# Kernel optimization log

Measured on AMD Instinct MI355X. Metric: run time of the kernel, lower is better.

The kernel has to match this reference:

```python
import jax, jax.numpy as jnp
import numpy as np

N = 100000
E = 1600000
NEG_SLOPE = 0.2


def gat_layer(x, W, al, ar, b, src, dst):
    """DGL GATConv (no dropout, no residual, bias=True, activation=None).
    x: [N, in]; W: [in, H*D]; al, ar, b: [H, D]. Returns [N, H, D]."""
    H, D = al.shape
    feat = (x @ W).reshape(N, H, D)               # [N,H,D]
    el = jnp.sum(feat * al, axis=-1)              # [N,H]
    er = jnp.sum(feat * ar, axis=-1)              # [N,H]
    e = jax.nn.leaky_relu(el[src] + er[dst], NEG_SLOPE)  # [E,H]
    # segment softmax over incoming edges of each dst node
    emax = jax.lax.stop_gradient(jax.ops.segment_max(e, dst, num_segments=N))
    ex = jnp.exp(e - emax[dst])                   # [E,H]
    denom = jax.ops.segment_sum(ex, dst, num_segments=N)  # [N,H]
    alpha = ex / jnp.where(denom[dst] == 0, 1.0, denom[dst])  # [E,H]
    msg = feat[src] * alpha[..., None]            # [E,H,D] gather + weight
    out = jax.ops.segment_sum(msg, dst, num_segments=N)    # [N,H,D] scatter-add
    return out + b[None, :, :]


def setup_inputs() -> dict:
    key = jax.random.key(0)
    ks = jax.random.split(key, 12)
    in_size, hid, out_size, heads = 128, 32, 16, 4
    x = jax.random.normal(ks[0], (N, in_size), dtype=jnp.float32)
    src = jax.random.randint(ks[1], (E,), 0, N, dtype=jnp.int32)
    dst = jax.random.randint(ks[2], (E,), 0, N, dtype=jnp.int32)
    W1 = jax.random.normal(ks[3], (in_size, heads * hid), dtype=jnp.float32) * (1.0 / np.sqrt(in_size))
    al1 = jax.random.normal(ks[4], (heads, hid), dtype=jnp.float32) * 0.1
    ar1 = jax.random.normal(ks[5], (heads, hid), dtype=jnp.float32) * 0.1
    b1 = jnp.zeros((heads, hid), dtype=jnp.float32)
    W2 = jax.random.normal(ks[6], (hid, out_size), dtype=jnp.float32) * (1.0 / np.sqrt(hid))
    al2 = jax.random.normal(ks[7], (1, out_size), dtype=jnp.float32) * 0.1
    ar2 = jax.random.normal(ks[8], (1, out_size), dtype=jnp.float32) * 0.1
    b2 = jnp.zeros((1, out_size), dtype=jnp.float32)
    return {"x": x, "src": src, "dst": dst, "W1": W1, "al1": al1, "ar1": ar1,
            "b1": b1, "W2": W2, "al2": al2, "ar2": ar2, "b2": b2}


def reference(x, src, dst, W1, al1, ar1, b1, W2, al2, ar2, b2):
    h = gat_layer(x, W1, al1, ar1, b1, src, dst)   # [N, heads, hid]
    h = jax.nn.relu(jnp.mean(h, axis=1))           # mean over heads + relu
    h = gat_layer(h, W2, al2, ar2, b2, src, dst)   # [N, 1, out]
    return h.reshape(N, -1)                        # flatten
```

## Files before the change

kernel.cpp:

```cpp
#include <hip/hip_runtime.h>
#include <hip/hip_bf16.h>

#define NEG_SLOPE 0.2f
#define LOG2E 1.44269504f
#define G_SHIFT 7
#define GSZ 128
#define CHUNK 4096

typedef __attribute__((ext_vector_type(8))) __bf16 bf16x8;
typedef __attribute__((ext_vector_type(4))) float f32x4;
typedef __attribute__((ext_vector_type(2))) float f32x2;

__device__ __forceinline__ unsigned short f2bf(float f) {
    unsigned u = __float_as_uint(f);
    unsigned r = (u + 0x7fffu + ((u >> 16) & 1u)) >> 16;
    return (unsigned short)r;
}
__device__ __forceinline__ float bflo(unsigned v) { return __uint_as_float(v << 16); }
__device__ __forceinline__ float bfhi(unsigned v) { return __uint_as_float(v & 0xffff0000u); }
__device__ __forceinline__ float bf2f(unsigned short v) {
    return __uint_as_float((unsigned)v << 16);
}

__global__ __launch_bounds__(256) void coarse_scatter(
    const int* __restrict__ src, const int* __restrict__ dst,
    int* __restrict__ gcursor, unsigned* __restrict__ inter, int NB, int E) {
    __shared__ int hist[800];
    __shared__ int lbase[800];
    __shared__ int gbase[800];
    __shared__ unsigned stage[CHUNK];
    __shared__ unsigned short bstage[CHUNK];

    const int tid = threadIdx.x;
    const int e0 = blockIdx.x * CHUNK;
    const int cnt = min(CHUNK, E - e0);

    for (int i = tid; i < NB; i += 256) hist[i] = 0;
    __syncthreads();

    unsigned pk[16];
    int bb[16];
    unsigned short rk[16];
#pragma unroll
    for (int r = 0; r < 16; ++r) {
        int idx = tid + r * 256;
        if (idx < cnt) {
            int s = src[e0 + idx];
            int d = dst[e0 + idx];
            pk[r] = ((unsigned)s << G_SHIFT) | (unsigned)(d & (GSZ - 1));
            bb[r] = d >> G_SHIFT;
            rk[r] = (unsigned short)atomicAdd(&hist[bb[r]], 1);
        }
    }
    __syncthreads();
    if (tid < 64) {
        int carry = 0;
        for (int i = 0; i < NB; i += 64) {
            int v = (i + tid < NB) ? hist[i + tid] : 0;
            int xv = v;
            for (int o = 1; o < 64; o <<= 1) {
                int tt = __shfl_up(xv, o, 64);
                if (tid >= o) xv += tt;
            }
            if (i + tid < NB) lbase[i + tid] = carry + xv - v;
            carry += __shfl(xv, 63, 64);
        }
    }
    __syncthreads();
    for (int i = tid; i < NB; i += 256) {
        int hh = hist[i];
        gbase[i] = (hh > 0) ? (i * CHUNK + atomicAdd(&gcursor[i], hh)) : 0;
    }
    __syncthreads();
#pragma unroll
    for (int r = 0; r < 16; ++r) {
        int idx = tid + r * 256;
        if (idx < cnt) {
            int pos = lbase[bb[r]] + (int)rk[r];
            stage[pos] = pk[r];
            bstage[pos] = (unsigned short)bb[r];
        }
    }
    __syncthreads();
#pragma unroll
    for (int r = 0; r < 16; ++r) {
        int idx = tid + r * 256;
        if (idx < cnt) {
            int b = (int)bstage[idx];
            inter[gbase[b] + (idx - lbase[b])] = stage[idx];
        }
    }
}

__global__ __launch_bounds__(256) void fine_scatter(
    const unsigned* __restrict__ inter, const int* __restrict__ gcursor,
    int* __restrict__ deg, int* __restrict__ rowptr, int* __restrict__ esrc,
    int N, int NB) {
    __shared__ int h[GSZ];
    __shared__ int lb[GSZ];
    __shared__ int redsum[256];
    const int b = blockIdx.x;
    const int tid = threadIdx.x;
    const int cnt = gcursor[b];
    const unsigned* ep = inter + (size_t)b * CHUNK;

    {
        int s = 0;
        for (int i = tid; i < b; i += 256) s += gcursor[i];
        redsum[tid] = s;
        __syncthreads();
        for (int o = 128; o > 0; o >>= 1) {
            if (tid < o) redsum[tid] += redsum[tid + o];
            __syncthreads();
        }
    }
    const int base = redsum[0];

    if (tid < GSZ) h[tid] = 0;
    __syncthreads();

    for (int idx = tid; idx < cnt; idx += 256)
        atomicAdd(&h[(int)(ep[idx] & (GSZ - 1))], 1);
    __syncthreads();

    if (tid < 64) {
        int carry = 0;
        for (int i = 0; i < GSZ; i += 64) {
            int v = h[i + tid];
            int xv = v;
            for (int o = 1; o < 64; o <<= 1) {
                int tt = __shfl_up(xv, o, 64);
                if (tid >= o) xv += tt;
            }
            lb[i + tid] = carry + xv - v;
            carry += __shfl(xv, 63, 64);
        }
    }
    __syncthreads();
    if (tid < GSZ) {
        int node = b * GSZ + tid;
        if (node < N) {
            deg[node] = h[tid];
            rowptr[node] = base + lb[tid];
        }
        h[tid] = 0;
    }
    __syncthreads();

    int* eb = esrc + base;
    for (int idx = tid; idx < cnt; idx += 256) {
        unsigned ed = ep[idx];
        int l = (int)(ed & (GSZ - 1));
        int rk = atomicAdd(&h[l], 1);
        eb[lb[l] + rk] = (int)(ed >> G_SHIFT);
    }
}

__global__ __launch_bounds__(128) void wconv_kernel(
    const float* __restrict__ W, unsigned short* __restrict__ wtb) {
    int c = blockIdx.x;
    int k = threadIdx.x;
    wtb[c * 128 + k] = f2bf(W[k * 128 + c]);
}

#define GSTRIDE 136
__global__ __launch_bounds__(256) void gemm1_mfma(
    const float* __restrict__ x, const unsigned short* __restrict__ wtb,
    const float* __restrict__ al, const float* __restrict__ ar,
    unsigned short* __restrict__ featb, float* __restrict__ el,
    float* __restrict__ er, int N) {
    __shared__ unsigned short xs[128][GSTRIDE];
    __shared__ unsigned short ws[128][GSTRIDE];
    const int t = threadIdx.x;
    const int m0 = blockIdx.x * 128;
    const int w = t >> 6;
    const int l = t & 63;
    const int lr = l & 15;
    const int lg = l >> 4;

    {
        const uint4* wv = (const uint4*)wtb;
#pragma unroll
        for (int rr = 0; rr < 8; ++rr) {
            int q = t + 256 * rr;
            int c = q >> 4, kb = q & 15;
            uint4 v = wv[q];
            *((uint4*)&ws[c][kb * 8]) = v;
        }
    }
    {
#pragma unroll
        for (int rr = 0; rr < 16; ++rr) {
            int q = t + 256 * rr;
            int row = q >> 5, c4 = q & 31;
            int gm = m0 + row;
            if (gm >= N) gm = N - 1;
            float4 v = *((const float4*)(x + (size_t)gm * 128 + c4 * 4));
            ushort4 o;
            o.x = f2bf(v.x); o.y = f2bf(v.y); o.z = f2bf(v.z); o.w = f2bf(v.w);
            *((ushort4*)&xs[row][c4 * 4]) = o;
        }
    }
    __syncthreads();

    f32x4 acc[2][8];
#pragma unroll
    for (int i = 0; i < 2; ++i)
#pragma unroll
        for (int j = 0; j < 8; ++j) acc[i][j] = (f32x4){0.f, 0.f, 0.f, 0.f};

#pragma unroll
    for (int kk = 0; kk < 4; ++kk) {
        const int k0 = kk * 32 + lg * 8;
        bf16x8 a0 = *((const bf16x8*)&xs[w * 32 + lr][k0]);
        bf16x8 a1 = *((const bf16x8*)&xs[w * 32 + 16 + lr][k0]);
#pragma unroll
        for (int nj = 0; nj < 8; ++nj) {
            bf16x8 bfr = *((const bf16x8*)&ws[nj * 16 + lr][k0]);
            acc[0][nj] = __builtin_amdgcn_mfma_f32_16x16x32_bf16(a0, bfr, acc[0][nj], 0, 0, 0);
            acc[1][nj] = __builtin_amdgcn_mfma_f32_16x16x32_bf16(a1, bfr, acc[1][nj], 0, 0, 0);
        }
    }
    __syncthreads();
#pragma unroll
    for (int mi = 0; mi < 2; ++mi)
#pragma unroll
        for (int r = 0; r < 4; ++r) {
            int row = w * 32 + mi * 16 + lg * 4 + r;
#pragma unroll
            for (int nj = 0; nj < 8; ++nj)
                xs[row][nj * 16 + lr] = f2bf(acc[mi][nj][r]);
        }
    __syncthreads();
    {
        int row = t >> 1, half = t & 1;
        int gm = m0 + row;
        if (gm < N) {
            float pl0 = 0.f, pl1 = 0.f, pr0 = 0.f, pr1 = 0.f;
            const unsigned short* xr = &xs[row][half * 64];
            uint4* outp = (uint4*)(featb + (size_t)gm * 128 + half * 64);
#pragma unroll
            for (int b8 = 0; b8 < 8; ++b8) {
                uint4 v = *((const uint4*)(xr + b8 * 8));
                int cb = half * 64 + b8 * 8;
                float4 a0 = *((const float4*)(al + cb));
                float4 a1 = *((const float4*)(al + cb + 4));
                float4 r0 = *((const float4*)(ar + cb));
                float4 r1 = *((const float4*)(ar + cb + 4));
                float f0 = bflo(v.x), f1 = bfhi(v.x), f2 = bflo(v.y), f3 = bfhi(v.y);
                float f4 = bflo(v.z), f5 = bfhi(v.z), f6 = bflo(v.w), f7 = bfhi(v.w);
                float sl = f0 * a0.x + f1 * a0.y + f2 * a0.z + f3 * a0.w
                         + f4 * a1.x + f5 * a1.y + f6 * a1.z + f7 * a1.w;
                float sr = f0 * r0.x + f1 * r0.y + f2 * r0.z + f3 * r0.w
                         + f4 * r1.x + f5 * r1.y + f6 * r1.z + f7 * r1.w;
                if (b8 < 4) { pl0 += sl; pr0 += sr; } else { pl1 += sl; pr1 += sr; }
                outp[b8] = v;
            }
            el[gm * 4 + half * 2 + 0] = pl0 * LOG2E;
            el[gm * 4 + half * 2 + 1] = pl1 * LOG2E;
            er[gm * 4 + half * 2 + 0] = pr0 * LOG2E;
            er[gm * 4 + half * 2 + 1] = pr1 * LOG2E;
        }
    }
}

__global__ __launch_bounds__(256) void pull1_kernel(
    const int* __restrict__ rowptr, const int* __restrict__ deg,
    const int* __restrict__ esrc, const float* __restrict__ el,
    const float* __restrict__ er, const unsigned short* __restrict__ featb,
    const float* __restrict__ b,
    const float* __restrict__ W2, const float* __restrict__ al2,
    const float* __restrict__ ar2, unsigned short* __restrict__ feat2b,
    float* __restrict__ el2, float* __restrict__ er2, int N) {
    int tid = blockIdx.x * 256 + threadIdx.x;
    int node = tid >> 4;
    int lane = threadIdx.x & 15;
    if (node >= N) return;
    int h = lane >> 2;
    int dq = lane & 3;
    int start = rowptr[node];
    int cnt = deg[node];
    float er_nh = er[node * 4 + h];
    const int* ep = esrc + start;
    const unsigned short* fb = featb + h * 32 + dq * 8;

    f32x2 acc2[4];
#pragma unroll
    for (int j = 0; j < 4; ++j) acc2[j] = (f32x2){0.f, 0.f};
    float sumex = 0.f;

    for (int i = 0; i < cnt; i += 8) {
        int s[8]; float e[8]; uint4 u[8];
#pragma unroll
        for (int j = 0; j < 8; ++j) {
            int idx = i + j;
            idx = (idx < cnt) ? idx : (cnt - 1);
            s[j] = ep[idx];
        }
#pragma unroll
        for (int j = 0; j < 8; ++j) u[j] = *((const uint4*)(fb + (size_t)s[j] * 128));
#pragma unroll
        for (int j = 0; j < 8; ++j) e[j] = el[s[j] * 4 + h];
#pragma unroll
        for (int j = 0; j < 8; ++j) {
            float v = e[j] + er_nh;
            v = fmaxf(v, NEG_SLOPE * v);
            float xx = (i + j < cnt) ? exp2f(v) : 0.f;
            sumex += xx;
            f32x2 xx2 = (f32x2){xx, xx};
            acc2[0] += xx2 * (f32x2){bflo(u[j].x), bfhi(u[j].x)};
            acc2[1] += xx2 * (f32x2){bflo(u[j].y), bfhi(u[j].y)};
            acc2[2] += xx2 * (f32x2){bflo(u[j].z), bfhi(u[j].z)};
            acc2[3] += xx2 * (f32x2){bflo(u[j].w), bfhi(u[j].w)};
        }
    }

    float inv = 1.f / ((sumex == 0.f) ? 1.f : sumex);
    float4 bb0 = *((const float4*)(b + h * 32 + dq * 8));
    float4 bb1 = *((const float4*)(b + h * 32 + dq * 8 + 4));
    float o[8];
    o[0] = acc2[0].x * inv + bb0.x; o[1] = acc2[0].y * inv + bb0.y;
    o[2] = acc2[1].x * inv + bb0.z; o[3] = acc2[1].y * inv + bb0.w;
    o[4] = acc2[2].x * inv + bb1.x; o[5] = acc2[2].y * inv + bb1.y;
    o[6] = acc2[3].x * inv + bb1.z; o[7] = acc2[3].y * inv + bb1.w;
#pragma unroll
    for (int j = 0; j < 8; ++j) {
        o[j] += __shfl_xor(o[j], 4);
        o[j] += __shfl_xor(o[j], 8);
        o[j] = fmaxf(o[j] * 0.25f, 0.f);
    }
    int c = lane;
    float fc = 0.f;
#pragma unroll
    for (int q = 0; q < 4; ++q) {
#pragma unroll
        for (int j = 0; j < 8; ++j) {
            float hv = __shfl(o[j], q, 16);
            fc += hv * W2[(q * 8 + j) * 16 + c];
        }
    }
    float pl = fc * al2[c];
    float pr = fc * ar2[c];
    pl += __shfl_xor(pl, 1); pl += __shfl_xor(pl, 2);
    pl += __shfl_xor(pl, 4); pl += __shfl_xor(pl, 8);
    pr += __shfl_xor(pr, 1); pr += __shfl_xor(pr, 2);
    pr += __shfl_xor(pr, 4); pr += __shfl_xor(pr, 8);
    feat2b[(size_t)node * 16 + c] = f2bf(fc);
    if (lane == 0) {
        el2[node] = pl * LOG2E;
        er2[node] = pr * LOG2E;
    }
}

__global__ __launch_bounds__(128) void pull2_kernel(
    const int* __restrict__ rowptr, const int* __restrict__ deg,
    const int* __restrict__ esrc, const float* __restrict__ el,
    const float* __restrict__ er, const unsigned short* __restrict__ feat2b,
    const float* __restrict__ b, float* __restrict__ outp, int N) {
    int tid = blockIdx.x * 128 + threadIdx.x;
    int node = tid >> 2;
    int d4 = threadIdx.x & 3;
    if (node >= N) return;

    int start = rowptr[node];
    int cnt = deg[node];
    float er_n = er[node];
    const int* ep = esrc + start;
    const unsigned short* fb = feat2b + d4 * 4;

    f32x2 acc01 = (f32x2){0.f, 0.f};
    f32x2 acc23 = (f32x2){0.f, 0.f};
    float sumex = 0.f;
    for (int i = 0; i < cnt; i += 8) {
        int s[8]; float ee[8]; ushort4 ff[8];
#pragma unroll
        for (int j = 0; j < 8; ++j) {
            int idx = i + j;
            idx = (idx < cnt) ? idx : (cnt - 1);
            s[j] = ep[idx];
        }
#pragma unroll
        for (int j = 0; j < 8; ++j) {
            ee[j] = el[s[j]];
            ff[j] = *((const ushort4*)(fb + (size_t)s[j] * 16));
        }
#pragma unroll
        for (int j = 0; j < 8; ++j) {
            float v = ee[j] + er_n;
            v = fmaxf(v, NEG_SLOPE * v);
            float ex = (i + j < cnt) ? exp2f(v) : 0.f;
            sumex += ex;
            f32x2 ex2 = (f32x2){ex, ex};
            acc01 += ex2 * (f32x2){bf2f(ff[j].x), bf2f(ff[j].y)};
            acc23 += ex2 * (f32x2){bf2f(ff[j].z), bf2f(ff[j].w)};
        }
    }
    float inv = 1.f / ((sumex == 0.f) ? 1.f : sumex);
    float4 bb = *((const float4*)(b + d4 * 4));
    float4 o;
    o.x = acc01.x * inv + bb.x;
    o.y = acc01.y * inv + bb.y;
    o.z = acc23.x * inv + bb.z;
    o.w = acc23.y * inv + bb.w;
    *((float4*)(outp + (size_t)node * 16 + d4 * 4)) = o;
}

extern "C" void kernel_launch(void* const* d_in, const int* in_sizes, int n_in,
                              void* d_out, int out_size, void* d_ws, size_t ws_size,
                              hipStream_t stream) {
    const float* x   = (const float*)d_in[0];
    const int*   src = (const int*)d_in[1];
    const int*   dst = (const int*)d_in[2];
    const float* W1  = (const float*)d_in[3];
    const float* al1 = (const float*)d_in[4];
    const float* ar1 = (const float*)d_in[5];
    const float* b1  = (const float*)d_in[6];
    const float* W2  = (const float*)d_in[7];
    const float* al2 = (const float*)d_in[8];
    const float* ar2 = (const float*)d_in[9];
    const float* b2  = (const float*)d_in[10];

    const int E = in_sizes[1];
    const int N = in_sizes[0] / 128;
    const int H1 = 4, C1 = 128;
    const int D2 = 16;
    const int NB = (N + GSZ - 1) / GSZ;
    const int NCH = (E + CHUNK - 1) / CHUNK;

    char* p = (char*)d_ws;
    auto alloc_f = [&](size_t n) { float* q = (float*)p; p += n * sizeof(float); return q; };
    auto alloc_i = [&](size_t n) { int* q = (int*)p; p += n * sizeof(int); return q; };

    unsigned short* feat1b = (unsigned short*)p; p += (size_t)N * C1 * sizeof(unsigned short);
    unsigned short* feat2b = (unsigned short*)p; p += (size_t)N * D2 * sizeof(unsigned short);
    float* el1   = alloc_f((size_t)N * H1);
    float* er1   = alloc_f((size_t)N * H1);
    float* el2   = alloc_f(N);
    float* er2   = alloc_f(N);
    int* deg     = alloc_i(N);
    int* rowptr  = alloc_i(N);
    int* esrc    = alloc_i(E);
    int* gcursor = alloc_i(NB);
    unsigned* inter = (unsigned*)alloc_i((size_t)NB * CHUNK);
    unsigned short* wtb = (unsigned short*)p; p += (size_t)128 * 128 * sizeof(unsigned short);

    const int TB = 256;

    hipMemsetAsync(gcursor, 0, (size_t)NB * sizeof(int), stream);
    wconv_kernel<<<128, 128, 0, stream>>>(W1, wtb);
    coarse_scatter<<<NCH, TB, 0, stream>>>(src, dst, gcursor, inter, NB, E);
    fine_scatter<<<NB, TB, 0, stream>>>(inter, gcursor, deg, rowptr, esrc, N, NB);

    gemm1_mfma<<<(N + 127) / 128, TB, 0, stream>>>(x, wtb, al1, ar1, feat1b, el1, er1, N);
    pull1_kernel<<<(int)(((long long)N * 16 + 255) / 256), TB, 0, stream>>>(
        rowptr, deg, esrc, el1, er1, feat1b, b1,
        W2, al2, ar2, feat2b, el2, er2, N);

    pull2_kernel<<<(int)(((long long)N * 4 + 127) / 128), 128, 0, stream>>>(
        rowptr, deg, esrc, el2, er2, feat2b, b2, (float*)d_out, N);
}
```

Baseline: 256.6 us.

## Merge independent preprocessing kernels and widen gather batches in pull kernels

The weight bf16 conversion moves into extra blocks of the coarse scatter kernel. The fine scatter moves into extra blocks of the GEMM kernel, which now shares one dynamic shared buffer between the two block roles. This cuts the launch count from four to two and lets independent work run concurrently. Both pull kernels now batch 16 neighbor gathers per iteration instead of 8 to raise memory-level parallelism, at the cost of more registers and more wasted clamped loads on low-degree nodes.

```diff
diff --git a/kernel.cpp b/kernel.cpp
--- a/kernel.cpp
+++ b/kernel.cpp
@@ -6,6 +6,7 @@
 #define G_SHIFT 7
 #define GSZ 128
 #define CHUNK 4096
+#define GSTRIDE 136
 
 typedef __attribute__((ext_vector_type(8))) __bf16 bf16x8;
 typedef __attribute__((ext_vector_type(4))) float f32x4;
@@ -22,9 +23,11 @@
     return __uint_as_float((unsigned)v << 16);
 }
 
-__global__ __launch_bounds__(256) void coarse_scatter(
+__global__ __launch_bounds__(256) void k1_scatter_wconv(
     const int* __restrict__ src, const int* __restrict__ dst,
-    int* __restrict__ gcursor, unsigned* __restrict__ inter, int NB, int E) {
+    int* __restrict__ gcursor, unsigned* __restrict__ inter,
+    const float* __restrict__ W, unsigned short* __restrict__ wtb,
+    int NB, int E, int NCH) {
     __shared__ int hist[800];
     __shared__ int lbase[800];
     __shared__ int gbase[800];
@@ -32,6 +35,13 @@
     __shared__ unsigned short bstage[CHUNK];
 
     const int tid = threadIdx.x;
+    if ((int)blockIdx.x >= NCH) {
+        int idx = ((int)blockIdx.x - NCH) * 256 + tid;
+        int c = idx >> 7, k = idx & 127;
+        wtb[idx] = f2bf(W[k * 128 + c]);
+        return;
+    }
+
     const int e0 = blockIdx.x * CHUNK;
     const int cnt = min(CHUNK, E - e0);
 
@@ -92,87 +102,78 @@
     }
 }
 
-__global__ __launch_bounds__(256) void fine_scatter(
+__global__ __launch_bounds__(256) void k2_fine_gemm(
     const unsigned* __restrict__ inter, const int* __restrict__ gcursor,
     int* __restrict__ deg, int* __restrict__ rowptr, int* __restrict__ esrc,
-    int N, int NB) {
-    __shared__ int h[GSZ];
-    __shared__ int lb[GSZ];
-    __shared__ int redsum[256];
-    const int b = blockIdx.x;
-    const int tid = threadIdx.x;
-    const int cnt = gcursor[b];
-    const unsigned* ep = inter + (size_t)b * CHUNK;
-
-    {
-        int s = 0;
-        for (int i = tid; i < b; i += 256) s += gcursor[i];
-        redsum[tid] = s;
-        __syncthreads();
-        for (int o = 128; o > 0; o >>= 1) {
-            if (tid < o) redsum[tid] += redsum[tid + o];
-            __syncthreads();
-        }
-    }
-    const int base = redsum[0];
-
-    if (tid < GSZ) h[tid] = 0;
-    __syncthreads();
-
-    for (int idx = tid; idx < cnt; idx += 256)
-        atomicAdd(&h[(int)(ep[idx] & (GSZ - 1))], 1);
-    __syncthreads();
-
-    if (tid < 64) {
-        int carry = 0;
-        for (int i = 0; i < GSZ; i += 64) {
-            int v = h[i + tid];
-            int xv = v;
-            for (int o = 1; o < 64; o <<= 1) {
-                int tt = __shfl_up(xv, o, 64);
-                if (tid >= o) xv += tt;
-            }
-            lb[i + tid] = carry + xv - v;
-            carry += __shfl(xv, 63, 64);
-        }
-    }
-    __syncthreads();
-    if (tid < GSZ) {
-        int node = b * GSZ + tid;
-        if (node < N) {
-            deg[node] = h[tid];
-            rowptr[node] = base + lb[tid];
-        }
-        h[tid] = 0;
-    }
-    __syncthreads();
-
-    int* eb = esrc + base;
-    for (int idx = tid; idx < cnt; idx += 256) {
-        unsigned ed = ep[idx];
-        int l = (int)(ed & (GSZ - 1));
-        int rk = atomicAdd(&h[l], 1);
-        eb[lb[l] + rk] = (int)(ed >> G_SHIFT);
-    }
-}
-
-__global__ __launch_bounds__(128) void wconv_kernel(
-    const float* __restrict__ W, unsigned short* __restrict__ wtb) {
-    int c = blockIdx.x;
-    int k = threadIdx.x;
-    wtb[c * 128 + k] = f2bf(W[k * 128 + c]);
-}
-
-#define GSTRIDE 136
-__global__ __launch_bounds__(256) void gemm1_mfma(
     const float* __restrict__ x, const unsigned short* __restrict__ wtb,
     const float* __restrict__ al, const float* __restrict__ ar,
     unsigned short* __restrict__ featb, float* __restrict__ el,
-    float* __restrict__ er, int N) {
-    __shared__ unsigned short xs[128][GSTRIDE];
-    __shared__ unsigned short ws[128][GSTRIDE];
-    const int t = threadIdx.x;
-    const int m0 = blockIdx.x * 128;
+    float* __restrict__ er, int N, int NB) {
+    __shared__ __align__(16) unsigned short smem[2 * 128 * GSTRIDE];
+    const int tid = threadIdx.x;
+
+    if ((int)blockIdx.x < NB) {
+        int* h = (int*)smem;
+        int* lb = h + GSZ;
+        int* redsum = lb + GSZ;
+        const int b = blockIdx.x;
+        const int cnt = gcursor[b];
+        const unsigned* ep = inter + (size_t)b * CHUNK;
+
+        {
+            int s = 0;
+            for (int i = tid; i < b; i += 256) s += gcursor[i];
+            redsum[tid] = s;
+            __syncthreads();
+            for (int o = 128; o > 0; o >>= 1) {
+                if (tid < o) redsum[tid] += redsum[tid + o];
+                __syncthreads();
+            }
+        }
+        const int base = redsum[0];
+
+        if (tid < GSZ) h[tid] = 0;
+        __syncthreads();
+        for (int idx = tid; idx < cnt; idx += 256)
+            atomicAdd(&h[(int)(ep[idx] & (GSZ - 1))], 1);
+        __syncthreads();
+        if (tid < 64) {
+            int carry = 0;
+            for (int i = 0; i < GSZ; i += 64) {
+                int v = h[i + tid];
+                int xv = v;
+                for (int o = 1; o < 64; o <<= 1) {
+                    int tt = __shfl_up(xv, o, 64);
+                    if (tid >= o) xv += tt;
+                }
+                lb[i + tid] = carry + xv - v;
+                carry += __shfl(xv, 63, 64);
+            }
+        }
+        __syncthreads();
+        if (tid < GSZ) {
+            int node = b * GSZ + tid;
+            if (node < N) {
+                deg[node] = h[tid];
+                rowptr[node] = base + lb[tid];
+            }
+            h[tid] = 0;
+        }
+        __syncthreads();
+        int* eb = esrc + base;
+        for (int idx = tid; idx < cnt; idx += 256) {
+            unsigned ed = ep[idx];
+            int l = (int)(ed & (GSZ - 1));
+            int rk = atomicAdd(&h[l], 1);
+            eb[lb[l] + rk] = (int)(ed >> G_SHIFT);
+        }
+        return;
+    }
+
+    unsigned short (*xs)[GSTRIDE] = (unsigned short(*)[GSTRIDE])smem;
+    unsigned short (*ws)[GSTRIDE] = (unsigned short(*)[GSTRIDE])(smem + 128 * GSTRIDE);
+    const int t = tid;
+    const int m0 = ((int)blockIdx.x - NB) * 128;
     const int w = t >> 6;
     const int l = t & 63;
     const int lr = l & 15;
@@ -289,20 +290,22 @@
     for (int j = 0; j < 4; ++j) acc2[j] = (f32x2){0.f, 0.f};
     float sumex = 0.f;
 
-    for (int i = 0; i < cnt; i += 8) {
-        int s[8]; float e[8]; uint4 u[8];
-#pragma unroll
-        for (int j = 0; j < 8; ++j) {
+    for (int i = 0; i < cnt; i += 16) {
+        int s[16];
+#pragma unroll
+        for (int j = 0; j < 16; ++j) {
             int idx = i + j;
             idx = (idx < cnt) ? idx : (cnt - 1);
             s[j] = ep[idx];
         }
-#pragma unroll
-        for (int j = 0; j < 8; ++j) u[j] = *((const uint4*)(fb + (size_t)s[j] * 128));
-#pragma unroll
-        for (int j = 0; j < 8; ++j) e[j] = el[s[j] * 4 + h];
-#pragma unroll
-        for (int j = 0; j < 8; ++j) {
+        uint4 u[16];
+#pragma unroll
+        for (int j = 0; j < 16; ++j) u[j] = *((const uint4*)(fb + (size_t)s[j] * 128));
+        float e[16];
+#pragma unroll
+        for (int j = 0; j < 16; ++j) e[j] = el[s[j] * 4 + h];
+#pragma unroll
+        for (int j = 0; j < 16; ++j) {
             float v = e[j] + er_nh;
             v = fmaxf(v, NEG_SLOPE * v);
             float xx = (i + j < cnt) ? exp2f(v) : 0.f;
@@ -371,21 +374,22 @@
     f32x2 acc01 = (f32x2){0.f, 0.f};
     f32x2 acc23 = (f32x2){0.f, 0.f};
     float sumex = 0.f;
-    for (int i = 0; i < cnt; i += 8) {
-        int s[8]; float ee[8]; ushort4 ff[8];
-#pragma unroll
-        for (int j = 0; j < 8; ++j) {
+    for (int i = 0; i < cnt; i += 16) {
+        int s[16];
+#pragma unroll
+        for (int j = 0; j < 16; ++j) {
             int idx = i + j;
             idx = (idx < cnt) ? idx : (cnt - 1);
             s[j] = ep[idx];
         }
-#pragma unroll
-        for (int j = 0; j < 8; ++j) {
-            ee[j] = el[s[j]];
-            ff[j] = *((const ushort4*)(fb + (size_t)s[j] * 16));
-        }
-#pragma unroll
-        for (int j = 0; j < 8; ++j) {
+        ushort4 ff[16];
+#pragma unroll
+        for (int j = 0; j < 16; ++j) ff[j] = *((const ushort4*)(fb + (size_t)s[j] * 16));
+        float ee[16];
+#pragma unroll
+        for (int j = 0; j < 16; ++j) ee[j] = el[s[j]];
+#pragma unroll
+        for (int j = 0; j < 16; ++j) {
             float v = ee[j] + er_n;
             v = fmaxf(v, NEG_SLOPE * v);
             float ex = (i + j < cnt) ? exp2f(v) : 0.f;
@@ -426,6 +430,7 @@
     const int D2 = 16;
     const int NB = (N + GSZ - 1) / GSZ;
     const int NCH = (E + CHUNK - 1) / CHUNK;
+    const int GB = (N + 127) / 128;
 
     char* p = (char*)d_ws;
     auto alloc_f = [&](size_t n) { float* q = (float*)p; p += n * sizeof(float); return q; };
@@ -447,11 +452,13 @@
     const int TB = 256;
 
     hipMemsetAsync(gcursor, 0, (size_t)NB * sizeof(int), stream);
-    wconv_kernel<<<128, 128, 0, stream>>>(W1, wtb);
-    coarse_scatter<<<NCH, TB, 0, stream>>>(src, dst, gcursor, inter, NB, E);
-    fine_scatter<<<NB, TB, 0, stream>>>(inter, gcursor, deg, rowptr, esrc, N, NB);
-
-    gemm1_mfma<<<(N + 127) / 128, TB, 0, stream>>>(x, wtb, al1, ar1, feat1b, el1, er1, N);
+    k1_scatter_wconv<<<NCH + 64, TB, 0, stream>>>(
+        src, dst, gcursor, inter, W1, wtb, NB, E, NCH);
+
+    k2_fine_gemm<<<NB + GB, TB, 0, stream>>>(
+        inter, gcursor, deg, rowptr, esrc,
+        x, wtb, al1, ar1, feat1b, el1, er1, N, NB);
+
     pull1_kernel<<<(int)(((long long)N * 16 + 255) / 256), TB, 0, stream>>>(
         rowptr, deg, esrc, el1, er1, feat1b, b1,
         W2, al2, ar2, feat2b, el2, er2, N);
```

After: 251.6 us. -2.0%, faster.
